# Optimization experiments

Measured on AMD Instinct MI355X. Metric: run time of the kernel, lower is better.

## Reference

```python
import jax, jax.numpy as jnp
import numpy as np

B, WK, HRS = 2048, 52, 8760
DT = 0.125          # Euler step in days (3-hourly), exactly representable
RANGE_PRED = 7      # forecast horizon in days


def setup_inputs() -> dict:
    key = jax.random.key(0)
    k1, k2, k3, k4 = jax.random.split(key, 4)
    # X_in: [B, weeks, 5, 1]; channel 0 = start time in days (same across batch,
    # the torch code reads X_in[0, week, 0, 0]); channels 1..4 = N,P,Z,D init.
    X_in = jax.random.uniform(k1, (B, WK, 5, 1), jnp.float32, 0.1, 3.0)
    t0 = jnp.arange(WK, dtype=jnp.float32) * 7.0
    X_in = X_in.at[:, :, 0, 0].set(jnp.broadcast_to(t0, (B, WK)))
    global_f = jax.random.uniform(k2, (B, HRS), jnp.float32)          # light forcing in [0,1]
    global_m = jax.random.uniform(k3, (B, HRS), jnp.float32) * 0.1    # mixing rate, small
    params_value = jax.random.uniform(k4, (B, 10), jnp.float32, 0.1, 1.0)
    return {"X_in": X_in, "global_f": global_f, "global_m": global_m,
            "params_value": params_value, "dt": DT, "range_pred": RANGE_PRED}


def reference(X_in, global_f, global_m, params_value, dt, range_pred):
    # Fixed multipliers from the torch code
    pv = jnp.asarray([1.0, 2.0, 0.1, 0.05, 0.1, 0.3, 0.6, 0.15, 0.4, 0.1], X_in.dtype)
    Q0, Vm, thr = 8.0, 1.0, 0.01  # Q0 = 4 + 2.5 + 1.5 + 0
    chi, rho, gam, lam, eps, alp, bet, eta, phi, zet = [params_value[:, i][:, None] for i in range(10)]  # [B,1]

    n_steps = int(round(range_pred / dt))      # 56
    stride = int(round(1.0 / dt))              # 8 -> daily sampling of output

    # Hourly forcing gather: same time axis for every batch element (torch uses X_in[0,...])
    t0 = X_in[0, :, 0, 0]                                                     # [W]
    times = t0[:, None] + jnp.arange(n_steps + 1, dtype=X_in.dtype) * dt      # [W, S]
    idx = jnp.round(times * 24.0).astype(jnp.int32)
    f = jnp.take(global_f, idx, axis=1)[:, :, :n_steps]                       # [B, W, T]
    m = jnp.take(global_m, idx, axis=1)[:, :, :n_steps]

    def step(carry, ft_mt):
        N, P, Z, D = carry                      # each [B, W]
        ft, mt = ft_mt
        Pc = jnp.maximum(thr, P)
        Zc = jnp.maximum(thr, Z)
        gN = N / (chi * pv[0] + N)
        zg = rho * pv[1] * (1.0 - jnp.exp(-lam * pv[3] * Pc)) * Zc
        up = Vm * gN * ft * Pc
        Nn = N + dt * (-up + alp * pv[5] * zg + eps * pv[4] * P + gam * pv[2] * Z + phi * pv[8] * D + mt * (Q0 - N))
        Pn = P + dt * (up - zg - eps * pv[4] * P - eta * pv[7] * P - mt * P)
        Zn = Z + dt * (bet * pv[6] * zg - gam * pv[2] * Z - mt * Z)
        Dn = D + dt * (eta * pv[7] * P + (1.0 - alp * pv[5] - bet * pv[6]) * zg - phi * pv[8] * D - zet * pv[9] * D - mt * D)
        new = (Nn, Pn, Zn, Dn)
        return new, jnp.stack(new, axis=0)      # [4, B, W]

    carry0 = (X_in[:, :, 1, 0], X_in[:, :, 2, 0], X_in[:, :, 3, 0], X_in[:, :, 4, 0])
    _, ys = jax.lax.scan(step, carry0, (jnp.moveaxis(f, 2, 0), jnp.moveaxis(m, 2, 0)))  # ys: [T, 4, B, W]
    traj = jnp.concatenate([jnp.stack(carry0, axis=0)[None], ys], axis=0)               # [S, 4, B, W]
    out = jnp.moveaxis(traj, (0, 1), (3, 2))                                            # [B, W, 4, S]
    return out[:, :, :, ::stride]               # daily samples: [B, W, 4, range_pred+1]
```

## Files before the change

kernel.cpp:

```cpp
#include <hip/hip_runtime.h>
#include <hip/hip_bf16.h>


#define NPZD_B 2048
#define NPZD_WK 52
#define NPZD_HRS 8760
#define NPZD_NSTEPS 56
#define NPZD_NK 2912
#define NPZD_GRP 208
#define NPZD_LDSW 3072

__global__ __launch_bounds__(256) void npzd_kernel(
    const float* __restrict__ X_in,
    const float* __restrict__ gf,
    const float* __restrict__ gm,
    const float* __restrict__ params,
    const float* __restrict__ dt_ptr,
    float* __restrict__ out)
{
    __shared__ float lds_f[NPZD_LDSW];
    __shared__ float lds_m[NPZD_LDSW];

    const int b   = blockIdx.x;
    const int tid = threadIdx.x;

    const float* __restrict__ frow = gf + (size_t)b * NPZD_HRS;
    const float* __restrict__ mrow = gm + (size_t)b * NPZD_HRS;

    #pragma unroll
    for (int j = 0; j < 12; ++j) {
        const unsigned k = (unsigned)(j * 256 + tid);
        const unsigned g = k / 208u;
        const unsigned r = k - g * 208u;
        const unsigned w = r >> 2;
        const unsigned q = r & 3u;
        const unsigned off = w * 168u + g * 12u + q * 3u;
        const int wb = j * 256 + (tid & 192);
        __builtin_amdgcn_global_load_lds(
            (const __attribute__((address_space(1))) void*)(frow + off),
            (__attribute__((address_space(3))) void*)(lds_f + wb), 4, 0, 0);
        __builtin_amdgcn_global_load_lds(
            (const __attribute__((address_space(1))) void*)(mrow + off),
            (__attribute__((address_space(3))) void*)(lds_m + wb), 4, 0, 0);
    }
    __syncthreads();

    if (tid >= NPZD_WK) return;
    const int w = tid;

    const float dt = dt_ptr[0];

    const float* xb = X_in + ((size_t)b * NPZD_WK + w) * 5;
    float N = xb[1], P = xb[2], Z = xb[3], D = xb[4];

    const float* pp = params + (size_t)b * 10;
    const float chi   = pp[0];
    const float rho2  = pp[1] * 2.0f;
    const float gam1  = pp[2] * 0.1f;
    const float lam05 = pp[3] * 0.05f;
    const float eps1  = pp[4] * 0.1f;
    const float alp3  = pp[5] * 0.3f;
    const float bet6  = pp[6] * 0.6f;
    const float eta15 = pp[7] * 0.15f;
    const float phi4  = pp[8] * 0.4f;
    const float zet1  = pp[9] * 0.1f;
    const float rem   = 1.0f - alp3 - bet6;

    float oN[8], oP[8], oZ[8], oD[8];
    oN[0] = N; oP[0] = P; oZ[0] = Z; oD[0] = D;

    #pragma unroll
    for (int g = 0; g < 14; ++g) {
        const float4 f4 = *(const float4*)(lds_f + g * NPZD_GRP + w * 4);
        const float4 m4 = *(const float4*)(lds_m + g * NPZD_GRP + w * 4);
        const float fs[4] = {f4.x, f4.y, f4.z, f4.w};
        const float ms[4] = {m4.x, m4.y, m4.z, m4.w};
        #pragma unroll
        for (int q = 0; q < 4; ++q) {
            const float ft = fs[q], mt = ms[q];
            const float Pc = fmaxf(0.01f, P);
            const float Zc = fmaxf(0.01f, Z);
            const float gN = N * __builtin_amdgcn_rcpf(chi + N);
            const float zg = rho2 * (1.0f - __expf(-lam05 * Pc)) * Zc;
            const float up = gN * ft * Pc;
            const float Nn = N + dt * (-up + alp3 * zg + eps1 * P + gam1 * Z + phi4 * D + mt * (8.0f - N));
            const float Pn = P + dt * (up - zg - eps1 * P - eta15 * P - mt * P);
            const float Zn = Z + dt * (bet6 * zg - gam1 * Z - mt * Z);
            const float Dn = D + dt * (eta15 * P + rem * zg - phi4 * D - zet1 * D - mt * D);
            N = Nn; P = Pn; Z = Zn; D = Dn;
        }
        if (g & 1) {
            const int c = (g >> 1) + 1;
            oN[c] = N; oP[c] = P; oZ[c] = Z; oD[c] = D;
        }
    }

    float4* o4 = (float4*)(out + ((size_t)b * NPZD_WK + w) * 32);
    o4[0] = make_float4(oN[0], oN[1], oN[2], oN[3]);
    o4[1] = make_float4(oN[4], oN[5], oN[6], oN[7]);
    o4[2] = make_float4(oP[0], oP[1], oP[2], oP[3]);
    o4[3] = make_float4(oP[4], oP[5], oP[6], oP[7]);
    o4[4] = make_float4(oZ[0], oZ[1], oZ[2], oZ[3]);
    o4[5] = make_float4(oZ[4], oZ[5], oZ[6], oZ[7]);
    o4[6] = make_float4(oD[0], oD[1], oD[2], oD[3]);
    o4[7] = make_float4(oD[4], oD[5], oD[6], oD[7]);
}

extern "C" void kernel_launch(void* const* d_in, const int* in_sizes, int n_in,
                              void* d_out, int out_size, void* d_ws, size_t ws_size,
                              hipStream_t stream) {
    const float* X_in   = (const float*)d_in[0];
    const float* gf     = (const float*)d_in[1];
    const float* gm     = (const float*)d_in[2];
    const float* params = (const float*)d_in[3];
    const float* dt_ptr = (const float*)d_in[4];
    float* out = (float*)d_out;

    npzd_kernel<<<NPZD_B, 256, 0, stream>>>(X_in, gf, gm, params, dt_ptr, out);
}
```

Baseline: 180.7 us.

## Load full forcing rows with vector loads and scatter strided samples into LDS

Replaces the per-element 4-byte global_load_lds gather of every third hourly sample with coalesced 16-byte nontemporal loads of whole forcing rows held in registers. The needed samples are then scattered into a per-week LDS layout with a 60-float stride. Each week's 56 inputs become contiguous, so the compute loop reads consecutive float4s. The aim is to cut the number of load instructions and avoid the small, fragmented gather. The cost is extra register pressure, index arithmetic, and scalar LDS stores.

```diff
diff --git a/kernel.cpp b/kernel.cpp
--- a/kernel.cpp
+++ b/kernel.cpp
@@ -1,14 +1,16 @@
 #include <hip/hip_runtime.h>
 #include <hip/hip_bf16.h>
 
+
+typedef float f32x4 __attribute__((ext_vector_type(4)));
 
 #define NPZD_B 2048
 #define NPZD_WK 52
 #define NPZD_HRS 8760
 #define NPZD_NSTEPS 56
-#define NPZD_NK 2912
-#define NPZD_GRP 208
-#define NPZD_LDSW 3072
+#define NPZD_NF4 2190
+#define NPZD_WSTRIDE 60
+#define NPZD_LDSW (NPZD_WK * NPZD_WSTRIDE + 16)
 
 __global__ __launch_bounds__(256) void npzd_kernel(
     const float* __restrict__ X_in,
@@ -18,30 +20,43 @@
     const float* __restrict__ dt_ptr,
     float* __restrict__ out)
 {
-    __shared__ float lds_f[NPZD_LDSW];
-    __shared__ float lds_m[NPZD_LDSW];
+    __shared__ __align__(16) float lds_f[NPZD_LDSW];
+    __shared__ __align__(16) float lds_m[NPZD_LDSW];
 
     const int b   = blockIdx.x;
     const int tid = threadIdx.x;
 
-    const float* __restrict__ frow = gf + (size_t)b * NPZD_HRS;
-    const float* __restrict__ mrow = gm + (size_t)b * NPZD_HRS;
+    const f32x4* __restrict__ gf4 = (const f32x4*)(gf + (size_t)b * NPZD_HRS);
+    const f32x4* __restrict__ gm4 = (const f32x4*)(gm + (size_t)b * NPZD_HRS);
+
+    f32x4 fv[9], mv[9];
+    int kk[9];
+    #pragma unroll
+    for (int i = 0; i < 9; ++i) {
+        int k = i * 256 + tid;
+        if (k >= NPZD_NF4) k = NPZD_NF4 - 1;
+        kk[i] = k;
+        fv[i] = __builtin_nontemporal_load(gf4 + k);
+        mv[i] = __builtin_nontemporal_load(gm4 + k);
+    }
 
     #pragma unroll
-    for (int j = 0; j < 12; ++j) {
-        const unsigned k = (unsigned)(j * 256 + tid);
-        const unsigned g = k / 208u;
-        const unsigned r = k - g * 208u;
-        const unsigned w = r >> 2;
-        const unsigned q = r & 3u;
-        const unsigned off = w * 168u + g * 12u + q * 3u;
-        const int wb = j * 256 + (tid & 192);
-        __builtin_amdgcn_global_load_lds(
-            (const __attribute__((address_space(1))) void*)(frow + off),
-            (__attribute__((address_space(3))) void*)(lds_f + wb), 4, 0, 0);
-        __builtin_amdgcn_global_load_lds(
-            (const __attribute__((address_space(1))) void*)(mrow + off),
-            (__attribute__((address_space(3))) void*)(lds_m + wb), 4, 0, 0);
+    for (int i = 0; i < 9; ++i) {
+        const int k = kk[i];
+        const float fe[4] = {fv[i].x, fv[i].y, fv[i].z, fv[i].w};
+        const float me[4] = {mv[i].x, mv[i].y, mv[i].z, mv[i].w};
+        const int rm = k % 3;
+        const int e0 = (rm == 0) ? 0 : (3 - rm);
+        const int j0 = (4 * k + e0) / 3;
+        const int p0 = j0 + 4 * ((j0 * 9363) >> 19);
+        lds_f[p0] = fe[e0];
+        lds_m[p0] = me[e0];
+        if (rm == 0) {
+            const int j1 = j0 + 1;
+            const int p1 = j1 + 4 * ((j1 * 9363) >> 19);
+            lds_f[p1] = fe[3];
+            lds_m[p1] = me[3];
+        }
     }
     __syncthreads();
 
@@ -69,10 +84,13 @@
     float oN[8], oP[8], oZ[8], oD[8];
     oN[0] = N; oP[0] = P; oZ[0] = Z; oD[0] = D;
 
+    const float* lf = lds_f + w * NPZD_WSTRIDE;
+    const float* lm = lds_m + w * NPZD_WSTRIDE;
+
     #pragma unroll
     for (int g = 0; g < 14; ++g) {
-        const float4 f4 = *(const float4*)(lds_f + g * NPZD_GRP + w * 4);
-        const float4 m4 = *(const float4*)(lds_m + g * NPZD_GRP + w * 4);
+        const f32x4 f4 = *(const f32x4*)(lf + 4 * g);
+        const f32x4 m4 = *(const f32x4*)(lm + 4 * g);
         const float fs[4] = {f4.x, f4.y, f4.z, f4.w};
         const float ms[4] = {m4.x, m4.y, m4.z, m4.w};
         #pragma unroll
@@ -95,15 +113,15 @@
         }
     }
 
-    float4* o4 = (float4*)(out + ((size_t)b * NPZD_WK + w) * 32);
-    o4[0] = make_float4(oN[0], oN[1], oN[2], oN[3]);
-    o4[1] = make_float4(oN[4], oN[5], oN[6], oN[7]);
-    o4[2] = make_float4(oP[0], oP[1], oP[2], oP[3]);
-    o4[3] = make_float4(oP[4], oP[5], oP[6], oP[7]);
-    o4[4] = make_float4(oZ[0], oZ[1], oZ[2], oZ[3]);
-    o4[5] = make_float4(oZ[4], oZ[5], oZ[6], oZ[7]);
-    o4[6] = make_float4(oD[0], oD[1], oD[2], oD[3]);
-    o4[7] = make_float4(oD[4], oD[5], oD[6], oD[7]);
+    f32x4* o4 = (f32x4*)(out + ((size_t)b * NPZD_WK + w) * 32);
+    o4[0] = (f32x4){oN[0], oN[1], oN[2], oN[3]};
+    o4[1] = (f32x4){oN[4], oN[5], oN[6], oN[7]};
+    o4[2] = (f32x4){oP[0], oP[1], oP[2], oP[3]};
+    o4[3] = (f32x4){oP[4], oP[5], oP[6], oP[7]};
+    o4[4] = (f32x4){oZ[0], oZ[1], oZ[2], oZ[3]};
+    o4[5] = (f32x4){oZ[4], oZ[5], oZ[6], oZ[7]};
+    o4[6] = (f32x4){oD[0], oD[1], oD[2], oD[3]};
+    o4[7] = (f32x4){oD[4], oD[5], oD[6], oD[7]};
 }
 
 extern "C" void kernel_launch(void* const* d_in, const int* in_sizes, int n_in,
```

Result: faster. 170.9 us (-5.4%).
